# Kernel tuning notes

Measured on AMD Instinct MI355X. Metric: run time of the kernel, lower is better.

The kernel has to match this reference:

```python
import jax, jax.numpy as jnp
import numpy as np

B, S, D, H = 4, 2048, 512, 8
DH = D // H  # depth per head = 64


def setup_inputs() -> dict:
    key = jax.random.key(0)
    ks = jax.random.split(key, 8)
    scale = 1.0 / np.sqrt(D)
    return {
        "query": jax.random.normal(ks[0], (B, S, D), jnp.float32),
        "key": jax.random.normal(ks[1], (B, S, D), jnp.float32),
        "value": jax.random.normal(ks[2], (B, S, D), jnp.float32),
        "mask": jax.random.randint(ks[3], (B, S), 0, 2, jnp.int32),
        "wq_w": jax.random.normal(ks[4], (D, D), jnp.float32) * scale,
        "wq_b": jnp.zeros((D,), jnp.float32),
        "wk_w": jax.random.normal(ks[5], (D, D), jnp.float32) * scale,
        "wk_b": jnp.zeros((D,), jnp.float32),
        "wv_w": jax.random.normal(ks[6], (D, D), jnp.float32) * scale,
        "wv_b": jnp.zeros((D,), jnp.float32),
        "wo_w": jax.random.normal(ks[7], (D, D), jnp.float32) * scale,
        "wo_b": jnp.zeros((D,), jnp.float32),
    }


def _split_heads(x):
    # [B, S, D] -> [B, H, S, DH]
    b, s, _ = x.shape
    return x.reshape(b, s, H, DH).transpose(0, 2, 1, 3)


def reference(query, key, value, mask, wq_w, wq_b, wk_w, wk_b, wv_w, wv_b, wo_w, wo_b):
    q = _split_heads(query @ wq_w + wq_b)   # [B,H,S,DH]
    k = _split_heads(key @ wk_w + wk_b)
    v = _split_heads(value @ wv_w + wv_b)

    scale = 1.0 / jnp.sqrt(jnp.asarray(DH, jnp.float32))
    logits = jnp.einsum('bhqd,bhkd->bhqk', q, k) * scale  # [B,H,S,S]
    # additive key-padding mask: 1 -> masked (adds -1e9)
    m = mask.astype(logits.dtype)[:, None, None, :]  # [B,1,1,S]
    logits = logits + m * -1e9
    weights = jax.nn.softmax(logits, axis=-1)
    attn = jnp.einsum('bhqk,bhkd->bhqd', weights, v)  # [B,H,S,DH]
    attn = attn.transpose(0, 2, 1, 3).reshape(query.shape[0], -1, D)  # [B,S,D]
    return attn @ wo_w + wo_b
```

## Files before the change

### kernel.cpp

```cpp
#include <hip/hip_runtime.h>
#include <stdint.h>

#define QSCALE (0.125f * 1.44269504088896340736f)
#define MASKNEG (-1.442695e9f)

typedef unsigned short u16;
typedef unsigned int u32;
typedef __bf16 bf16x8 __attribute__((ext_vector_type(8)));
typedef float f32x4 __attribute__((ext_vector_type(4)));
typedef float f32x16 __attribute__((ext_vector_type(16)));
typedef u16 u16x8 __attribute__((ext_vector_type(8)));
typedef u32 u32x4 __attribute__((ext_vector_type(4)));

__device__ __forceinline__ u16 f2bf(float f) {
  u32 u = __float_as_uint(f);
  u += 0x7fffu + ((u >> 16) & 1u);
  return (u16)(u >> 16);
}

__device__ __forceinline__ u32 cvtpk(float lo, float hi) {
  u32 d;
  asm("v_cvt_pk_bf16_f32 %0, %1, %2" : "=v"(d) : "v"(lo), "v"(hi));
  return d;
}

__device__ __forceinline__ void plswap(u32& a, u32& b) {
  asm("v_permlane32_swap_b32 %0, %1" : "+v"(a), "+v"(b));
}

__device__ __forceinline__ void gload16(const void* src, void* ldsbase) {
  __builtin_amdgcn_global_load_lds(
      (const __attribute__((address_space(1))) u32*)src,
      (__attribute__((address_space(3))) u32*)ldsbase, 16, 0, 0);
}

__global__ __launch_bounds__(256) void conv_w(const float* __restrict__ wq,
                                              const float* __restrict__ wk,
                                              const float* __restrict__ wv,
                                              const float* __restrict__ wo,
                                              u16* __restrict__ wT) {
  const float* src = (blockIdx.z == 0) ? wq : (blockIdx.z == 1) ? wk
                    : (blockIdx.z == 2) ? wv : wo;
  u16* dst = wT + (size_t)blockIdx.z * 262144;
  __shared__ float t[64][65];
  const int n0 = blockIdx.x * 64, k0 = blockIdx.y * 64;
  const int lr = threadIdx.x >> 6, lc = threadIdx.x & 63;
#pragma unroll
  for (int it = 0; it < 16; ++it) {
    const int row = it * 4 + lr;
    t[row][lc] = src[(size_t)(k0 + row) * 512 + n0 + lc];
  }
  __syncthreads();
#pragma unroll
  for (int it = 0; it < 16; ++it) {
    const int row = it * 4 + lr;
    dst[(size_t)(n0 + row) * 512 + k0 + lc] = f2bf(t[lc][row]);
  }
}

__global__ __launch_bounds__(512, 6) void gemm_qkv(
    const float* __restrict__ xqf, const float* __restrict__ xkf,
    const float* __restrict__ xvf, const u16* __restrict__ wT,
    const float* __restrict__ bq, const float* __restrict__ bk,
    const float* __restrict__ bv, u16* __restrict__ qws, u16* __restrict__ kws,
    u16* __restrict__ vTw) {
  __shared__ __align__(16) char lds[49152];
  const int hw = blockIdx.x;
  const int lg = (hw & 7) * 96 + (hw >> 3);
  const int z = lg >> 8;
  const int rem = lg & 255;
  const int m0 = (rem >> 2) * 128, n0 = (rem & 3) * 128;
  const float* A = (z == 0) ? xqf : (z == 1) ? xkf : xvf;
  const u16* Bt = wT + (size_t)z * 262144;
  const float* bias = (z == 0) ? bq : (z == 1) ? bk : bv;

  const int tid = threadIdx.x;
  const int lane = tid & 63;
  const int wave = tid >> 6;
  const int wm = wave >> 1, wn = wave & 1;
  const int h4 = lane >> 4, l15 = lane & 15;

  f32x4 acc[2][4] = {};

  auto stage = [&](int buf, int kt) {
    const int k0 = kt * 32;
    char* baseA = lds + buf * 24576;
    char* baseB = baseA + 16384;
    {
      const int sxA = tid & 7;
#pragma unroll
      for (int c = 0; c < 2; ++c) {
        const int row = c * 64 + (tid >> 3);
        const int sx = sxA ^ (row & 7);
        gload16(A + (size_t)(m0 + row) * 512 + k0 + sx * 4,
                baseA + c * 8192 + (wave << 10));
      }
    }
    {
      const int row = tid >> 2;
      const int sx = (tid & 3) ^ ((row ^ (row >> 2)) & 3);
      gload16(Bt + (size_t)(n0 + row) * 512 + k0 + sx * 8,
              baseB + (wave << 10));
    }
  };

  auto compute = [&](int buf) {
    const char* bA = lds + buf * 24576;
    const char* bB = bA + 16384;
    bf16x8 av[2], bv[4];
#pragma unroll
    for (int i = 0; i < 2; ++i) {
      const int row = wm * 32 + i * 16 + l15;
      const f32x4 lo =
          *(const f32x4*)(bA + row * 128 + (((h4 * 2) ^ (row & 7)) << 4));
      const f32x4 hi =
          *(const f32x4*)(bA + row * 128 + (((h4 * 2 + 1) ^ (row & 7)) << 4));
      u32x4 w;
      w[0] = cvtpk(lo[0], lo[1]);
      w[1] = cvtpk(lo[2], lo[3]);
      w[2] = cvtpk(hi[0], hi[1]);
      w[3] = cvtpk(hi[2], hi[3]);
      av[i] = __builtin_bit_cast(bf16x8, w);
    }
#pragma unroll
    for (int j = 0; j < 4; ++j) {
      const int row = wn * 64 + j * 16 + l15;
      bv[j] = *(const bf16x8*)(bB + row * 64 +
                               ((h4 ^ ((row ^ (row >> 2)) & 3)) << 4));
    }
#pragma unroll
    for (int i = 0; i < 2; ++i)
#pragma unroll
      for (int j = 0; j < 4; ++j)
        acc[i][j] = __builtin_amdgcn_mfma_f32_16x16x32_bf16(av[i], bv[j],
                                                            acc[i][j], 0, 0, 0);
  };

  stage(0, 0);
  __syncthreads();
#pragma unroll
  for (int kt = 0; kt < 16; ++kt) {
    const int cur = kt & 1;
    if (kt < 15) stage(cur ^ 1, kt + 1);
    compute(cur);
    __syncthreads();
  }

#pragma unroll
  for (int j = 0; j < 4; ++j) {
    const int n = n0 + wn * 64 + j * 16 + l15;
    const float bn = bias[n];
    const int h = n >> 6, dh = n & 63;
#pragma unroll
    for (int i = 0; i < 2; ++i) {
#pragma unroll
      for (int r = 0; r < 4; ++r) {
        const int rg = m0 + wm * 32 + i * 16 + h4 * 4 + r;
        const int b = rg >> 11, s = rg & 2047;
        const int bh = b * 8 + h;
        const float val = acc[i][j][r] + bn;
        if (z == 0) {
          qws[((size_t)bh * 2048 + s) * 64 + dh] = f2bf(val * QSCALE);
        } else if (z == 1) {
          kws[((size_t)bh * 2048 + s) * 64 + dh] = f2bf(val);
        } else {
          vTw[((size_t)bh * 64 + dh) * 2048 + s] = f2bf(val);
        }
      }
    }
  }
}

__global__ __launch_bounds__(512, 4) void attn_fwd(
    const u16* __restrict__ qws, const u16* __restrict__ kws,
    const u16* __restrict__ vTw, const int* __restrict__ mask,
    u16* __restrict__ attn) {
  __shared__ __align__(16) char ldsK[32768];
  __shared__ __align__(16) char ldsV[32768];
  __shared__ __align__(16) float biasLDS[2048];
  __shared__ float lShA[128];

  const int bh = blockIdx.x;
  const int qt = blockIdx.y;
  const int b = bh >> 3;
  const int tid = threadIdx.x;
  const int lane = tid & 63, wave = tid >> 6;
  const int half = wave >> 2, wl = wave & 3;
  const int l31 = lane & 31, h5 = lane >> 5;

  {
    const int4 m4 = *(const int4*)(mask + b * 2048 + tid * 4);
    float4 bv;
    bv.x = m4.x ? MASKNEG : 0.0f;
    bv.y = m4.y ? MASKNEG : 0.0f;
    bv.z = m4.z ? MASKNEG : 0.0f;
    bv.w = m4.w ? MASKNEG : 0.0f;
    *(float4*)(biasLDS + tid * 4) = bv;
  }
  asm volatile("s_waitcnt lgkmcnt(0)" ::: "memory");

  const u16* qrow_p = qws + ((size_t)bh * 2048 + qt * 128 + wl * 32 + l31) * 64;
  bf16x8 qb[4];
#pragma unroll
  for (int c = 0; c < 4; ++c)
    qb[c] = *(const bf16x8*)(qrow_p + c * 16 + h5 * 8);

  const int rowb = l31 * 128;
  const int tl = (l31 ^ (l31 >> 3)) & 7;
  int kxs[4];
#pragma unroll
  for (int c = 0; c < 4; ++c) kxs[c] = ((2 * c + h5) ^ tl) << 4;

  char* myK = ldsK + half * 16384;
  char* myV = ldsV + half * 16384;
  const int srow = wl * 8 + (lane >> 3);
  const int sc16 = lane & 7;

  auto stage = [&](int buf, int ktg) {
#pragma unroll
    for (int c = 0; c < 2; ++c) {
      const int row = c * 32 + srow;
      const int xc = (sc16 ^ ((row ^ (row >> 3)) & 7)) << 3;
      gload16(kws + ((size_t)bh * 2048 + ktg * 64 + row) * 64 + xc,
              myK + buf * 8192 + c * 4096 + (wl << 10));
      gload16(vTw + ((size_t)bh * 64 + row) * 2048 + ktg * 64 + xc,
              myV + buf * 8192 + c * 4096 + (wl << 10));
    }
  };

  f32x16 o0 = {}, o1 = {};
  float rsp0 = 0.f, rsp1 = 0.f, rsp2 = 0.f, rsp3 = 0.f;

  auto do_subtile = [&](const char* kb, const char* vb, const float* biasT,
                        int stByte, int c0) {
    const int xadj = stByte ? 64 : 0;
    f32x16 sv;
#pragma unroll
    for (int g = 0; g < 4; ++g) {
      const f32x4 bq4 = *(const f32x4*)(biasT + g * 8 + h5 * 4);
      sv[g * 4 + 0] = bq4[0];
      sv[g * 4 + 1] = bq4[1];
      sv[g * 4 + 2] = bq4[2];
      sv[g * 4 + 3] = bq4[3];
    }
    __builtin_amdgcn_s_setprio(1);
#pragma unroll
    for (int c = 0; c < 4; ++c) {
      const bf16x8 kf = *(const bf16x8*)(kb + stByte + rowb + (kxs[c] ^ xadj));
      sv = __builtin_amdgcn_mfma_f32_32x32x16_bf16(kf, qb[c], sv, 0, 0, 0);
    }
    __builtin_amdgcn_s_setprio(0);
    float p[16];
#pragma unroll
    for (int i = 0; i < 16; ++i) p[i] = __builtin_amdgcn_exp2f(sv[i]);
    rsp0 += p[0] + p[4] + p[8] + p[12];
    rsp1 += p[1] + p[5] + p[9] + p[13];
    rsp2 += p[2] + p[6] + p[10] + p[14];
    rsp3 += p[3] + p[7] + p[11] + p[15];
    u32 paw[2][4];
#pragma unroll
    for (int lc = 0; lc < 2; ++lc) {
      u32 a1 = cvtpk(p[lc * 8 + 0], p[lc * 8 + 1]);
      u32 b1 = cvtpk(p[lc * 8 + 4], p[lc * 8 + 5]);
      u32 a2 = cvtpk(p[lc * 8 + 2], p[lc * 8 + 3]);
      u32 b2 = cvtpk(p[lc * 8 + 6], p[lc * 8 + 7]);
      plswap(a1, b1);
      plswap(a2, b2);
      paw[lc][0] = a1; paw[lc][1] = a2; paw[lc][2] = b1; paw[lc][3] = b2;
    }
    __builtin_amdgcn_s_setprio(1);
#pragma unroll
    for (int lc = 0; lc < 2; ++lc) {
      u32x4 w = {paw[lc][0], paw[lc][1], paw[lc][2], paw[lc][3]};
      const bf16x8 pa = __builtin_bit_cast(bf16x8, w);
      const bf16x8 vf0 = *(const bf16x8*)(vb + rowb + kxs[c0 + lc]);
      o0 = __builtin_amdgcn_mfma_f32_32x32x16_bf16(pa, vf0, o0, 0, 0, 0);
      const bf16x8 vf1 =
          *(const bf16x8*)(vb + 4096 + rowb + (kxs[c0 + lc] ^ 64));
      o1 = __builtin_amdgcn_mfma_f32_32x32x16_bf16(pa, vf1, o1, 0, 0, 0);
    }
    __builtin_amdgcn_s_setprio(0);
  };

  stage(0, half * 16);

  for (int kt = 0; kt < 16; ++kt) {
    const int cur = kt & 1;
    const int ktg = half * 16 + kt;
    if (kt < 15) {
      stage(cur ^ 1, ktg + 1);
      asm volatile("s_waitcnt vmcnt(4)" ::: "memory");
    } else {
      asm volatile("s_waitcnt vmcnt(0)" ::: "memory");
    }
    __builtin_amdgcn_sched_barrier(0);
    __builtin_amdgcn_s_barrier();
    const char* kb = myK + cur * 8192;
    const char* vb = myV + cur * 8192;
    const float* biasT = biasLDS + ktg * 64;
    do_subtile(kb, vb, biasT, 0, 0);
    do_subtile(kb, vb, biasT + 32, 4096, 2);
    __builtin_amdgcn_sched_barrier(0);
    __builtin_amdgcn_s_barrier();
  }

  float rs = (rsp0 + rsp1) + (rsp2 + rsp3);
  rs += __shfl_xor(rs, 32);

  float* oSh2 = (float*)ldsK;
  u16* trb = (u16*)ldsV;
  if (half == 1) {
#pragma unroll
    for (int reg = 0; reg < 16; ++reg) {
      oSh2[(wl * 32 + reg) * 64 + lane] = o0[reg];
      oSh2[(wl * 32 + 16 + reg) * 64 + lane] = o1[reg];
    }
    if (h5 == 0) lShA[wl * 32 + l31] = rs;
  }
  __syncthreads();
  if (half == 0) {
    const float ltot = rs + lShA[wl * 32 + l31];
    const float linv = 1.0f / ltot;
#pragma unroll
    for (int reg = 0; reg < 16; ++reg) {
      const int q = (reg & 3) + 8 * (reg >> 2) + 4 * h5;
      const float inv = __shfl(linv, q);
      const float v0 = (o0[reg] + oSh2[(wl * 32 + reg) * 64 + lane]) * inv;
      const float v1 = (o1[reg] + oSh2[(wl * 32 + 16 + reg) * 64 + lane]) * inv;
      trb[(wl * 32 + q) * 64 + l31] = f2bf(v0);
      trb[(wl * 32 + q) * 64 + 32 + l31] = f2bf(v1);
    }
  }
  __syncthreads();
  const int h = bh & 7;
#pragma unroll
  for (int i = 0; i < 2; ++i) {
    const int ii = tid + i * 512;
    const int row = ii >> 3;
    const int c8 = (ii & 7) * 8;
    const u16x8 vv = *(const u16x8*)(trb + row * 64 + c8);
    const int grow = b * 2048 + qt * 128 + row;
    *(u16x8*)(attn + (size_t)grow * 512 + h * 64 + c8) = vv;
  }
}

__global__ __launch_bounds__(256, 3) void gemm_out(const u16* __restrict__ attn,
                                                   const u16* __restrict__ woT,
                                                   const float* __restrict__ bo,
                                                   float* __restrict__ out) {
  __shared__ __align__(16) char lds[49152];
  const int hw = blockIdx.x;
  const int lg = (hw & 7) * 64 + (hw >> 3);
  const int m0 = (lg >> 2) * 64, n0 = (lg & 3) * 128;

  const int tid = threadIdx.x;
  const int lane = tid & 63;
  const int wave = tid >> 6;
  const int wm = wave >> 1, wn = wave & 1;
  const int srow = tid >> 3;
  const int sc16 = tid & 7;

  f32x4 acc[2][4] = {};

  auto stage = [&](int buf, int kt) {
    const int k0 = kt * 64;
    char* base = lds + buf * 24576;
#pragma unroll
    for (int c = 0; c < 2; ++c) {
      const int row = c * 32 + srow;
      const int xc = (sc16 ^ (row & 7)) << 3;
      gload16(attn + (size_t)(m0 + row) * 512 + k0 + xc,
              base + c * 4096 + (wave << 10));
    }
#pragma unroll
    for (int c = 0; c < 4; ++c) {
      const int row = c * 32 + srow;
      const int xc = (sc16 ^ (row & 7)) << 3;
      gload16(woT + (size_t)(n0 + row) * 512 + k0 + xc,
              base + 8192 + c * 4096 + (wave << 10));
    }
  };

  auto compute = [&](int buf) {
    const char* bA = lds + buf * 24576;
    const char* bB = bA + 8192;
#pragma unroll
    for (int kk = 0; kk < 2; ++kk) {
      const int c16 = kk * 4 + (lane >> 4);
      bf16x8 av[2], bv[4];
#pragma unroll
      for (int i = 0; i < 2; ++i) {
        const int row = wm * 32 + i * 16 + (lane & 15);
        av[i] = *(const bf16x8*)(bA + row * 128 + ((c16 ^ (row & 7)) << 4));
      }
#pragma unroll
      for (int j = 0; j < 4; ++j) {
        const int row = wn * 64 + j * 16 + (lane & 15);
        bv[j] = *(const bf16x8*)(bB + row * 128 + ((c16 ^ (row & 7)) << 4));
      }
#pragma unroll
      for (int i = 0; i < 2; ++i)
#pragma unroll
        for (int j = 0; j < 4; ++j)
          acc[i][j] = __builtin_amdgcn_mfma_f32_16x16x32_bf16(av[i], bv[j],
                                                              acc[i][j], 0, 0, 0);
    }
  };

  stage(0, 0);
  __syncthreads();
#pragma unroll
  for (int kt = 0; kt < 8; ++kt) {
    const int cur = kt & 1;
    if (kt < 7) stage(cur ^ 1, kt + 1);
    compute(cur);
    __syncthreads();
  }

#pragma unroll
  for (int j = 0; j < 4; ++j) {
    const int n = n0 + wn * 64 + j * 16 + (lane & 15);
    const float bn = bo[n];
#pragma unroll
    for (int i = 0; i < 2; ++i) {
      const int rbase = m0 + wm * 32 + i * 16 + ((lane >> 4) << 2);
#pragma unroll
      for (int r = 0; r < 4; ++r)
        out[(size_t)(rbase + r) * 512 + n] = acc[i][j][r] + bn;
    }
  }
}

extern "C" void kernel_launch(void* const* d_in, const int* in_sizes, int n_in,
                              void* d_out, int out_size, void* d_ws,
                              size_t ws_size, hipStream_t stream) {
  (void)in_sizes; (void)n_in; (void)out_size; (void)ws_size;
  const float* q = (const float*)d_in[0];
  const float* k = (const float*)d_in[1];
  const float* v = (const float*)d_in[2];
  const int* mask = (const int*)d_in[3];
  const float* wq = (const float*)d_in[4];
  const float* bq = (const float*)d_in[5];
  const float* wk = (const float*)d_in[6];
  const float* bk = (const float*)d_in[7];
  const float* wv = (const float*)d_in[8];
  const float* bv = (const float*)d_in[9];
  const float* wo = (const float*)d_in[10];
  const float* bo = (const float*)d_in[11];

  u16* attnb = (u16*)d_ws;
  u16* wT = attnb + 4194304;
  u16* qws = wT + 1048576;
  u16* kws = qws + 4194304;
  u16* vTw = kws + 4194304;
  float* out = (float*)d_out;

  conv_w<<<dim3(8, 8, 4), 256, 0, stream>>>(wq, wk, wv, wo, wT);
  gemm_qkv<<<768, 512, 0, stream>>>(q, k, v, wT, bq, bk, bv, qws, kws, vTw);
  attn_fwd<<<dim3(32, 16), 512, 0, stream>>>(qws, kws, vTw, mask, attnb);
  gemm_out<<<512, 256, 0, stream>>>(attnb, wT + 786432, bo, out);
}
```

Before: 100.8 us.

## Pre-convert QKV inputs to bf16 and restructure QKV GEMM with full-K LDS tiles

```diff
diff --git a/kernel.cpp b/kernel.cpp
--- a/kernel.cpp
+++ b/kernel.cpp
@@ -32,6 +32,21 @@
   __builtin_amdgcn_global_load_lds(
       (const __attribute__((address_space(1))) u32*)src,
       (__attribute__((address_space(3))) u32*)ldsbase, 16, 0, 0);
+}
+
+__global__ __launch_bounds__(256) void conv_in(const float* __restrict__ q,
+                                               const float* __restrict__ k,
+                                               const float* __restrict__ v,
+                                               u16* __restrict__ dst) {
+  const float* src = (blockIdx.z == 0) ? q : (blockIdx.z == 1) ? k : v;
+  u16* d = dst + (size_t)blockIdx.z * 4194304;
+  size_t i = ((size_t)blockIdx.x * 256 + threadIdx.x) * 8;
+  float4 a = *(const float4*)(src + i);
+  float4 b = *(const float4*)(src + i + 4);
+  u16x8 ov;
+  ov[0] = f2bf(a.x); ov[1] = f2bf(a.y); ov[2] = f2bf(a.z); ov[3] = f2bf(a.w);
+  ov[4] = f2bf(b.x); ov[5] = f2bf(b.y); ov[6] = f2bf(b.z); ov[7] = f2bf(b.w);
+  *(u16x8*)(d + i) = ov;
 }
 
 __global__ __launch_bounds__(256) void conv_w(const float* __restrict__ wq,
@@ -58,114 +73,69 @@
   }
 }
 
-__global__ __launch_bounds__(512, 6) void gemm_qkv(
-    const float* __restrict__ xqf, const float* __restrict__ xkf,
-    const float* __restrict__ xvf, const u16* __restrict__ wT,
+__global__ __launch_bounds__(256) void gemm_qkv(
+    const u16* __restrict__ xq, const u16* __restrict__ xk,
+    const u16* __restrict__ xv, const u16* __restrict__ wT,
     const float* __restrict__ bq, const float* __restrict__ bk,
     const float* __restrict__ bv, u16* __restrict__ qws, u16* __restrict__ kws,
     u16* __restrict__ vTw) {
-  __shared__ __align__(16) char lds[49152];
+  __shared__ __align__(16) char lds[131072];
   const int hw = blockIdx.x;
-  const int lg = (hw & 7) * 96 + (hw >> 3);
-  const int z = lg >> 8;
-  const int rem = lg & 255;
-  const int m0 = (rem >> 2) * 128, n0 = (rem & 3) * 128;
-  const float* A = (z == 0) ? xqf : (z == 1) ? xkf : xvf;
+  const int lg = (hw & 7) * 384 + (hw >> 3);
+  const int z = lg >> 10;
+  const int rem = lg & 1023;
+  const int m0 = (rem >> 3) * 64, n0 = (rem & 7) * 64;
+  const u16* A = (z == 0) ? xq : (z == 1) ? xk : xv;
   const u16* Bt = wT + (size_t)z * 262144;
   const float* bias = (z == 0) ? bq : (z == 1) ? bk : bv;
 
   const int tid = threadIdx.x;
   const int lane = tid & 63;
   const int wave = tid >> 6;
-  const int wm = wave >> 1, wn = wave & 1;
   const int h4 = lane >> 4, l15 = lane & 15;
-
-  f32x4 acc[2][4] = {};
-
-  auto stage = [&](int buf, int kt) {
-    const int k0 = kt * 32;
-    char* baseA = lds + buf * 24576;
-    char* baseB = baseA + 16384;
-    {
-      const int sxA = tid & 7;
-#pragma unroll
-      for (int c = 0; c < 2; ++c) {
-        const int row = c * 64 + (tid >> 3);
-        const int sx = sxA ^ (row & 7);
-        gload16(A + (size_t)(m0 + row) * 512 + k0 + sx * 4,
-                baseA + c * 8192 + (wave << 10));
-      }
-    }
-    {
-      const int row = tid >> 2;
-      const int sx = (tid & 3) ^ ((row ^ (row >> 2)) & 3);
-      gload16(Bt + (size_t)(n0 + row) * 512 + k0 + sx * 8,
-              baseB + (wave << 10));
-    }
-  };
-
-  auto compute = [&](int buf) {
-    const char* bA = lds + buf * 24576;
-    const char* bB = bA + 16384;
-    bf16x8 av[2], bv[4];
-#pragma unroll
-    for (int i = 0; i < 2; ++i) {
-      const int row = wm * 32 + i * 16 + l15;
-      const f32x4 lo =
-          *(const f32x4*)(bA + row * 128 + (((h4 * 2) ^ (row & 7)) << 4));
-      const f32x4 hi =
-          *(const f32x4*)(bA + row * 128 + (((h4 * 2 + 1) ^ (row & 7)) << 4));
-      u32x4 w;
-      w[0] = cvtpk(lo[0], lo[1]);
-      w[1] = cvtpk(lo[2], lo[3]);
-      w[2] = cvtpk(hi[0], hi[1]);
-      w[3] = cvtpk(hi[2], hi[3]);
-      av[i] = __builtin_bit_cast(bf16x8, w);
-    }
+  const int tl7 = l15 & 7;
+
+  char* ldsA = lds;
+  char* ldsB = lds + 65536;
+#pragma unroll
+  for (int i = 0; i < 16; ++i) {
+    const int row = i * 4 + wave;
+    const int sc = lane ^ (row & 7);
+    gload16(A + (size_t)(m0 + row) * 512 + sc * 8, ldsA + row * 1024);
+    gload16(Bt + (size_t)(n0 + row) * 512 + sc * 8, ldsB + row * 1024);
+  }
+  __syncthreads();
+
+  f32x4 acc[4] = {};
+  const int arowb = (wave * 16 + l15) * 1024;
+#pragma unroll
+  for (int kk = 0; kk < 16; ++kk) {
+    const int slot = ((kk * 4 + h4) ^ tl7) << 4;
+    const bf16x8 av = *(const bf16x8*)(ldsA + arowb + slot);
 #pragma unroll
     for (int j = 0; j < 4; ++j) {
-      const int row = wn * 64 + j * 16 + l15;
-      bv[j] = *(const bf16x8*)(bB + row * 64 +
-                               ((h4 ^ ((row ^ (row >> 2)) & 3)) << 4));
-    }
-#pragma unroll
-    for (int i = 0; i < 2; ++i)
-#pragma unroll
-      for (int j = 0; j < 4; ++j)
-        acc[i][j] = __builtin_amdgcn_mfma_f32_16x16x32_bf16(av[i], bv[j],
-                                                            acc[i][j], 0, 0, 0);
-  };
-
-  stage(0, 0);
-  __syncthreads();
-#pragma unroll
-  for (int kt = 0; kt < 16; ++kt) {
-    const int cur = kt & 1;
-    if (kt < 15) stage(cur ^ 1, kt + 1);
-    compute(cur);
-    __syncthreads();
+      const bf16x8 bv8 = *(const bf16x8*)(ldsB + (j * 16 + l15) * 1024 + slot);
+      acc[j] = __builtin_amdgcn_mfma_f32_16x16x32_bf16(av, bv8, acc[j], 0, 0, 0);
+    }
   }
 
 #pragma unroll
   for (int j = 0; j < 4; ++j) {
-    const int n = n0 + wn * 64 + j * 16 + l15;
+    const int n = n0 + j * 16 + l15;
     const float bn = bias[n];
     const int h = n >> 6, dh = n & 63;
 #pragma unroll
-    for (int i = 0; i < 2; ++i) {
-#pragma unroll
-      for (int r = 0; r < 4; ++r) {
-        const int rg = m0 + wm * 32 + i * 16 + h4 * 4 + r;
-        const int b = rg >> 11, s = rg & 2047;
-        const int bh = b * 8 + h;
-        const float val = acc[i][j][r] + bn;
-        if (z == 0) {
-          qws[((size_t)bh * 2048 + s) * 64 + dh] = f2bf(val * QSCALE);
-        } else if (z == 1) {
-          kws[((size_t)bh * 2048 + s) * 64 + dh] = f2bf(val);
-        } else {
-          vTw[((size_t)bh * 64 + dh) * 2048 + s] = f2bf(val);
-        }
+    for (int r = 0; r < 4; ++r) {
+      const int rg = m0 + wave * 16 + h4 * 4 + r;
+      const int b = rg >> 11, s = rg & 2047;
+      const int bh = b * 8 + h;
+      const float val = acc[j][r] + bn;
+      if (z == 0) {
+        qws[((size_t)bh * 2048 + s) * 64 + dh] = f2bf(val * QSCALE);
+      } else if (z == 1) {
+        kws[((size_t)bh * 2048 + s) * 64 + dh] = f2bf(val);
+      } else {
+        vTw[((size_t)bh * 64 + dh) * 2048 + s] = f2bf(val);
       }
     }
   }
@@ -448,15 +418,19 @@
   const float* wo = (const float*)d_in[10];
   const float* bo = (const float*)d_in[11];
 
-  u16* attnb = (u16*)d_ws;
-  u16* wT = attnb + 4194304;
+  u16* xq = (u16*)d_ws;
+  u16* xk = xq + 4194304;
+  u16* xv = xk + 4194304;
+  u16* wT = xv + 4194304;
   u16* qws = wT + 1048576;
   u16* kws = qws + 4194304;
   u16* vTw = kws + 4194304;
+  u16* attnb = xq;
   float* out = (float*)d_out;
 
+  conv_in<<<dim3(2048, 1, 3), 256, 0, stream>>>(q, k, v, xq);
   conv_w<<<dim3(8, 8, 4), 256, 0, stream>>>(wq, wk, wv, wo, wT);
-  gemm_qkv<<<768, 512, 0, stream>>>(q, k, v, wT, bq, bk, bv, qws, kws, vTw);
+  gemm_qkv<<<3072, 256, 0, stream>>>(xq, xk, xv, wT, bq, bk, bv, qws, kws, vTw);
   attn_fwd<<<dim3(32, 16), 512, 0, stream>>>(qws, kws, vTw, mask, attnb);
   gemm_out<<<512, 256, 0, stream>>>(attnb, wT + 786432, bo, out);
 }
```

New measurement: 132.2 us. +31.2%, slower.
